# Kernel optimization log

Measured on AMD Instinct MI355X. Metric: run time of the kernel, lower is better.

## Reference

```python
import jax, jax.numpy as jnp
import numpy as np

PYR = 40000
N_PV, N_OLM, N_BIST = 2100, 1800, 1200
N_SEPT = 100
DT = 1.0
E_EXC, E_INH = 3.0, -0.5


def _sparse_uniform(key, n_out, n_in, conn, w_max, no_autapse=False):
    km, kw = jax.random.split(key)
    mask = jax.random.uniform(km, (n_out, n_in)) < conn
    w = jnp.where(mask, jax.random.uniform(kw, (n_out, n_in)) * w_max, 0.0)
    if no_autapse:
        w = w * (1.0 - jnp.eye(n_out))
    return w.astype(jnp.float32)


def setup_inputs() -> dict:
    key = jax.random.key(0)
    ks = jax.random.split(key, 24)
    inp = {}
    inp['pyr_spikes'] = jax.random.randint(ks[0], (PYR,), 0, 2, dtype=jnp.int32)
    inp['septal_gaba'] = jax.random.uniform(ks[1], (N_SEPT,), dtype=jnp.float32)
    inp['external_exc'] = jax.random.uniform(ks[2], (N_PV,), dtype=jnp.float32)
    inp['prev_pv_spikes'] = (jax.random.uniform(ks[3], (N_PV,)) < 0.1).astype(jnp.float32)
    inp['prev_olm_spikes'] = (jax.random.uniform(ks[4], (N_OLM,)) < 0.1).astype(jnp.float32)
    inp['prev_pv_v_mem'] = jax.random.uniform(ks[5], (N_PV,), dtype=jnp.float32)
    inp['pv_v'] = jax.random.uniform(ks[6], (N_PV,), dtype=jnp.float32)
    inp['olm_v'] = jax.random.uniform(ks[7], (N_OLM,), dtype=jnp.float32)
    inp['bist_v'] = jax.random.uniform(ks[8], (N_BIST,), dtype=jnp.float32)
    inp['pv_adapt'] = jnp.zeros((N_PV,), jnp.float32)
    inp['olm_adapt'] = jnp.zeros((N_OLM,), jnp.float32)
    inp['bist_adapt'] = jnp.zeros((N_BIST,), jnp.float32)
    # weights per WeightInitializer.sparse_uniform calls in __init__ (ca1_inhibitory branch)
    inp['pyr_to_pv'] = _sparse_uniform(ks[9], N_PV, PYR, 0.5, 0.0012)
    inp['pyr_to_olm'] = _sparse_uniform(ks[10], N_OLM, PYR, 0.3, 0.0006)
    inp['pyr_to_bist'] = _sparse_uniform(ks[11], N_BIST, PYR, 0.35, 0.0007)
    inp['pv_to_pyr'] = _sparse_uniform(ks[12], PYR, N_PV, 0.5, 0.003)
    inp['pv_to_pyr_gaba_b'] = _sparse_uniform(ks[13], PYR, N_PV, 0.5, 0.003 * 0.15)
    inp['olm_to_pyr'] = _sparse_uniform(ks[14], PYR, N_OLM, 0.5, 0.001)
    inp['bist_to_pyr'] = _sparse_uniform(ks[15], PYR, N_BIST, 0.55, 0.002)
    inp['pv_to_pv'] = _sparse_uniform(ks[16], N_PV, N_PV, 0.3, 0.0005, no_autapse=True)
    inp['olm_to_pv'] = _sparse_uniform(ks[17], N_PV, N_OLM, 0.2, 0.0004)
    gj = _sparse_uniform(ks[18], N_PV, N_PV, 0.5, 0.0003, no_autapse=True)
    inp['pv_gap'] = (gj + gj.T) * 0.5  # symmetrized gap junctions
    inp['septal_to_olm'] = (jnp.abs(jax.random.normal(ks[19], (N_OLM, N_SEPT))) * 0.5).astype(jnp.float32)
    return inp


def _split_exc(g, nmda_ratio=0.3):
    g = jnp.maximum(g, 0.0)  # conductances are nonnegative
    return g * (1.0 - nmda_ratio), g * nmda_ratio


def _lif_step(v, adapt, g_ampa, g_nmda, g_gaba_a, tau_mem, v_th, v_reset, tau_adapt, adapt_inc):
    # conductance-based LIF: leak toward 0 (v_rest), synaptic currents toward reversals
    i_syn = (g_ampa + g_nmda) * (E_EXC - v) + g_gaba_a * (E_INH - v)
    v_new = v + (DT / tau_mem) * (-v + i_syn)
    spk = (v_new >= (v_th + adapt)).astype(v.dtype)
    v_out = jnp.where(spk > 0, v_reset, v_new)
    adapt_new = adapt * (1.0 - DT / tau_adapt) + adapt_inc * spk
    return spk, v_out, adapt_new


def reference(pyr_spikes, septal_gaba, external_exc, prev_pv_spikes, prev_olm_spikes,
              prev_pv_v_mem, pv_v, olm_v, bist_v, pv_adapt, olm_adapt, bist_adapt,
              pyr_to_pv, pyr_to_olm, pyr_to_bist, pv_to_pyr, pv_to_pyr_gaba_b,
              olm_to_pyr, bist_to_pyr, pv_to_pv, olm_to_pv, pv_gap, septal_to_olm):
    pyr_f = pyr_spikes.astype(jnp.float32)
    pv_exc = pyr_to_pv @ pyr_f
    olm_exc = pyr_to_olm @ pyr_f
    bist_exc = pyr_to_bist @ pyr_f
    pv_exc_from_pyr = pv_exc
    ext_mean = external_exc.mean()
    pv_exc = pv_exc + ext_mean * 0.3
    olm_exc = olm_exc + ext_mean * 0.1
    bist_exc = bist_exc + ext_mean * 0.2
    olm_g_inh = septal_to_olm @ septal_gaba
    pv_lateral = pv_to_pv @ prev_pv_spikes
    olm_to_pv_inhib = olm_to_pv @ prev_olm_spikes
    pv_exc = pv_exc - pv_lateral * 0.5 - olm_to_pv_inhib * 0.3
    # gap junctions: gated by mean pyramidal drive (traced condition -> where)
    drive = pv_exc_from_pyr.mean()
    gain = jnp.where(drive > 0.01, jnp.minimum(1.0, drive / 0.1), 0.0)
    pv_gap_current = pv_gap @ prev_pv_v_mem  # v @ W.T with symmetric-ish W
    pv_exc = pv_exc + pv_gap_current * 0.05 * gain
    pv_ga, pv_gn = _split_exc(pv_exc)
    olm_ga, olm_gn = _split_exc(olm_exc)
    bi_ga, bi_gn = _split_exc(bist_exc)
    zero_pv = jnp.zeros_like(pv_v)
    zero_bi = jnp.zeros_like(bist_v)
    pv_spk, _, _ = _lif_step(pv_v, pv_adapt, pv_ga, pv_gn, zero_pv, 7.0, 2.0, 0.0, 50.0, 0.05)
    olm_spk, _, _ = _lif_step(olm_v, olm_adapt, olm_ga, olm_gn, olm_g_inh, 25.0, 1.1, 0.0, 100.0, 0.2)
    bist_spk, _, _ = _lif_step(bist_v, bist_adapt, bi_ga, bi_gn, zero_bi, 12.0, 0.9, 0.0, 60.0, 0.08)
    perisomatic = pv_to_pyr @ pv_spk
    perisomatic_gaba_b = pv_to_pyr_gaba_b @ pv_spk
    olm_dendritic = olm_to_pyr @ olm_spk
    dendritic = olm_dendritic + bist_to_pyr @ bist_spk
    return (perisomatic, perisomatic_gaba_b, dendritic, olm_dendritic, pv_spk, olm_spk, bist_spk)
```

## Files before the change

kernel.cpp:

```cpp
#include <hip/hip_runtime.h>

#define PYR 40000
#define N_PV 2100
#define N_OLM 1800
#define N_BIST 1200
#define N_SEPT 100

#define WS_PV_RAW   0
#define WS_OLM_RAW  2100
#define WS_BIST_RAW 3900
#define WS_PV_LAT   5100
#define WS_OLM_IPV  7200
#define WS_GAP      9300
#define WS_OLM_GINH 11400
#define WS_SCAL     13200

#define O_PERI 0
#define O_GABA 40000
#define O_DEND 80000
#define O_OLMD 120000
#define O_PVS  160000
#define O_OLMS 162100
#define O_BIS  163900

__device__ __forceinline__ float wave_reduce(float acc) {
    #pragma unroll
    for (int o = 32; o > 0; o >>= 1) acc += __shfl_down(acc, o, 64);
    return acc;
}

__global__ __launch_bounds__(256) void k_phase1(
    const float* __restrict__ Wpv, const float* __restrict__ Wolm,
    const float* __restrict__ Wbi, const int* __restrict__ pyr,
    float* __restrict__ ws)
{
    int b = blockIdx.x;
    const float* W;
    float* dst;
    if (b < N_PV)               { W = Wpv  + (size_t)b * PYR;                 dst = ws + WS_PV_RAW  + b; }
    else if (b < N_PV + N_OLM)  { int r = b - N_PV;         W = Wolm + (size_t)r * PYR; dst = ws + WS_OLM_RAW  + r; }
    else                        { int r = b - N_PV - N_OLM; W = Wbi  + (size_t)r * PYR; dst = ws + WS_BIST_RAW + r; }

    const float4* W4 = (const float4*)W;
    const int4*   S4 = (const int4*)pyr;
    float acc = 0.0f;
    for (int j = threadIdx.x; j < PYR / 4; j += 256) {
        float4 w = W4[j];
        int4   s = S4[j];
        acc += w.x * (float)s.x + w.y * (float)s.y + w.z * (float)s.z + w.w * (float)s.w;
    }
    acc = wave_reduce(acc);
    __shared__ float sm[4];
    int lane = threadIdx.x & 63, wv = threadIdx.x >> 6;
    if (lane == 0) sm[wv] = acc;
    __syncthreads();
    if (threadIdx.x == 0) *dst = sm[0] + sm[1] + sm[2] + sm[3];
}

__global__ __launch_bounds__(256) void k_small(
    const float* __restrict__ Wpvpv, const float* __restrict__ Wolmpv,
    const float* __restrict__ Wgap,  const float* __restrict__ Wsept,
    const float* __restrict__ prev_pv, const float* __restrict__ prev_olm,
    const float* __restrict__ prev_vm, const float* __restrict__ sept_g,
    float* __restrict__ ws)
{
    int r = blockIdx.x * 4 + (threadIdx.x >> 6);
    int lane = threadIdx.x & 63;
    const float* W; const float* v; int len4; float* dst;
    if (r < N_PV)                   { W = Wpvpv  + (size_t)r * N_PV;              v = prev_pv;  len4 = N_PV / 4;  dst = ws + WS_PV_LAT  + r; }
    else if (r < 2 * N_PV)          { int i = r - N_PV;     W = Wolmpv + (size_t)i * N_OLM;  v = prev_olm; len4 = N_OLM / 4; dst = ws + WS_OLM_IPV + i; }
    else if (r < 3 * N_PV)          { int i = r - 2 * N_PV; W = Wgap   + (size_t)i * N_PV;   v = prev_vm;  len4 = N_PV / 4;  dst = ws + WS_GAP     + i; }
    else if (r < 3 * N_PV + N_OLM)  { int i = r - 3 * N_PV; W = Wsept  + (size_t)i * N_SEPT; v = sept_g;   len4 = N_SEPT / 4; dst = ws + WS_OLM_GINH + i; }
    else return;

    const float4* W4 = (const float4*)W;
    const float4* V4 = (const float4*)v;
    float acc = 0.0f;
    for (int j = lane; j < len4; j += 64) {
        float4 w = W4[j], x = V4[j];
        acc += w.x * x.x + w.y * x.y + w.z * x.z + w.w * x.w;
    }
    acc = wave_reduce(acc);
    if (lane == 0) *dst = acc;
}

__global__ __launch_bounds__(256) void k_scal(const float* __restrict__ ext, float* __restrict__ ws)
{
    __shared__ float s1[256], s2[256];
    float a = 0.0f, b = 0.0f;
    for (int i = threadIdx.x; i < N_PV; i += 256) { a += ext[i]; b += ws[WS_PV_RAW + i]; }
    s1[threadIdx.x] = a; s2[threadIdx.x] = b;
    __syncthreads();
    for (int o = 128; o > 0; o >>= 1) {
        if (threadIdx.x < o) { s1[threadIdx.x] += s1[threadIdx.x + o]; s2[threadIdx.x] += s2[threadIdx.x + o]; }
        __syncthreads();
    }
    if (threadIdx.x == 0) {
        float ext_mean = s1[0] / (float)N_PV;
        float drive    = s2[0] / (float)N_PV;
        float gain = (drive > 0.01f) ? fminf(1.0f, drive / 0.1f) : 0.0f;
        ws[WS_SCAL]     = ext_mean;
        ws[WS_SCAL + 1] = gain;
    }
}

__global__ __launch_bounds__(256) void k_lif(
    const float* __restrict__ ws,
    const float* __restrict__ pv_v,  const float* __restrict__ olm_v,  const float* __restrict__ bist_v,
    const float* __restrict__ pv_ad, const float* __restrict__ olm_ad, const float* __restrict__ bist_ad,
    float* __restrict__ out)
{
    int t = blockIdx.x * 256 + threadIdx.x;
    float ext_mean = ws[WS_SCAL], gain = ws[WS_SCAL + 1];
    if (t < N_PV) {
        float g = ws[WS_PV_RAW + t] + ext_mean * 0.3f
                - ws[WS_PV_LAT + t] * 0.5f - ws[WS_OLM_IPV + t] * 0.3f
                + ws[WS_GAP + t] * 0.05f * gain;
        g = fmaxf(g, 0.0f);
        float ga = g * 0.7f, gn = g * 0.3f;
        float v = pv_v[t], ad = pv_ad[t];
        float isyn = (ga + gn) * (3.0f - v);
        float vn = v + (1.0f / 7.0f) * (-v + isyn);
        out[O_PVS + t] = (vn >= 2.0f + ad) ? 1.0f : 0.0f;
    } else if (t < N_PV + N_OLM) {
        int i = t - N_PV;
        float g = ws[WS_OLM_RAW + i] + ext_mean * 0.1f;
        g = fmaxf(g, 0.0f);
        float ga = g * 0.7f, gn = g * 0.3f;
        float gi = ws[WS_OLM_GINH + i];
        float v = olm_v[i], ad = olm_ad[i];
        float isyn = (ga + gn) * (3.0f - v) + gi * (-0.5f - v);
        float vn = v + (1.0f / 25.0f) * (-v + isyn);
        out[O_OLMS + i] = (vn >= 1.1f + ad) ? 1.0f : 0.0f;
    } else if (t < N_PV + N_OLM + N_BIST) {
        int i = t - N_PV - N_OLM;
        float g = ws[WS_BIST_RAW + i] + ext_mean * 0.2f;
        g = fmaxf(g, 0.0f);
        float ga = g * 0.7f, gn = g * 0.3f;
        float v = bist_v[i], ad = bist_ad[i];
        float isyn = (ga + gn) * (3.0f - v);
        float vn = v + (1.0f / 12.0f) * (-v + isyn);
        out[O_BIS + i] = (vn >= 0.9f + ad) ? 1.0f : 0.0f;
    }
}

__global__ __launch_bounds__(256) void k_phase2(
    const float* __restrict__ Wpp, const float* __restrict__ Wppb,
    const float* __restrict__ Wop, const float* __restrict__ Wbp,
    float* __restrict__ out)
{
    int r = blockIdx.x * 4 + (threadIdx.x >> 6);
    int lane = threadIdx.x & 63;
    int job = r / PYR;
    int p = r - job * PYR;
    const float* W; const float* v; int len4; float* dst;
    if (job == 0)      { W = Wpp  + (size_t)p * N_PV;   v = out + O_PVS;  len4 = N_PV / 4;   dst = out + O_PERI + p; }
    else if (job == 1) { W = Wppb + (size_t)p * N_PV;   v = out + O_PVS;  len4 = N_PV / 4;   dst = out + O_GABA + p; }
    else if (job == 2) { W = Wop  + (size_t)p * N_OLM;  v = out + O_OLMS; len4 = N_OLM / 4;  dst = out + O_OLMD + p; }
    else               { W = Wbp  + (size_t)p * N_BIST; v = out + O_BIS;  len4 = N_BIST / 4; dst = out + O_DEND + p; }

    const float4* W4 = (const float4*)W;
    const float4* V4 = (const float4*)v;
    float acc = 0.0f;
    for (int j = lane; j < len4; j += 64) {
        float4 w = W4[j], x = V4[j];
        acc += w.x * x.x + w.y * x.y + w.z * x.z + w.w * x.w;
    }
    acc = wave_reduce(acc);
    if (lane == 0) *dst = acc;
}

__global__ __launch_bounds__(256) void k_add(float* __restrict__ out)
{
    int i = blockIdx.x * 256 + threadIdx.x;
    if (i < PYR) out[O_DEND + i] += out[O_OLMD + i];
}

extern "C" void kernel_launch(void* const* d_in, const int* in_sizes, int n_in,
                              void* d_out, int out_size, void* d_ws, size_t ws_size,
                              hipStream_t stream)
{
    const int*   pyr     = (const int*)  d_in[0];
    const float* sept_g  = (const float*)d_in[1];
    const float* ext     = (const float*)d_in[2];
    const float* prev_pv = (const float*)d_in[3];
    const float* prev_olm= (const float*)d_in[4];
    const float* prev_vm = (const float*)d_in[5];
    const float* pv_v    = (const float*)d_in[6];
    const float* olm_v   = (const float*)d_in[7];
    const float* bist_v  = (const float*)d_in[8];
    const float* pv_ad   = (const float*)d_in[9];
    const float* olm_ad  = (const float*)d_in[10];
    const float* bist_ad = (const float*)d_in[11];
    const float* Wpyr_pv = (const float*)d_in[12];
    const float* Wpyr_olm= (const float*)d_in[13];
    const float* Wpyr_bi = (const float*)d_in[14];
    const float* Wpp     = (const float*)d_in[15];
    const float* Wppb    = (const float*)d_in[16];
    const float* Wop     = (const float*)d_in[17];
    const float* Wbp     = (const float*)d_in[18];
    const float* Wpvpv   = (const float*)d_in[19];
    const float* Wolmpv  = (const float*)d_in[20];
    const float* Wgap    = (const float*)d_in[21];
    const float* Wsept   = (const float*)d_in[22];

    float* ws  = (float*)d_ws;
    float* out = (float*)d_out;

    k_phase1<<<N_PV + N_OLM + N_BIST, 256, 0, stream>>>(Wpyr_pv, Wpyr_olm, Wpyr_bi, pyr, ws);
    k_small<<<(3 * N_PV + N_OLM) / 4, 256, 0, stream>>>(Wpvpv, Wolmpv, Wgap, Wsept,
                                                        prev_pv, prev_olm, prev_vm, sept_g, ws);
    k_scal<<<1, 256, 0, stream>>>(ext, ws);
    k_lif<<<(N_PV + N_OLM + N_BIST + 255) / 256, 256, 0, stream>>>(
        ws, pv_v, olm_v, bist_v, pv_ad, olm_ad, bist_ad, out);
    k_phase2<<<(4 * PYR) / 4, 256, 0, stream>>>(Wpp, Wppb, Wop, Wbp, out);
    k_add<<<(PYR + 255) / 256, 256, 0, stream>>>(out);
}
```

Baseline: 368.7 us.

## Fuse launches, merge dendritic dot products, and use nontemporal weight loads

Merges the large pyramidal-input matvec kernel and the small recurrent matvec kernel into one launch. The scalar-mean reduction moves into the LIF kernel, where every block recomputes it redundantly. Phase 2 now computes the OLM and bistratified dot products in the same wave, so the separate add kernel goes away. Weight streams use nontemporal loads to avoid polluting cache. This removes three launches and an extra pass over the dendritic output, at the cost of redundant reductions and more divergent block types.

```diff
diff --git a/kernel.cpp b/kernel.cpp
--- a/kernel.cpp
+++ b/kernel.cpp
@@ -13,7 +13,6 @@
 #define WS_OLM_IPV  7200
 #define WS_GAP      9300
 #define WS_OLM_GINH 11400
-#define WS_SCAL     13200
 
 #define O_PERI 0
 #define O_GABA 40000
@@ -23,122 +22,113 @@
 #define O_OLMS 162100
 #define O_BIS  163900
 
+typedef float f4 __attribute__((ext_vector_type(4)));
+typedef int   i4 __attribute__((ext_vector_type(4)));
+
+__device__ __forceinline__ f4 ntload(const f4* p) { return __builtin_nontemporal_load(p); }
+
 __device__ __forceinline__ float wave_reduce(float acc) {
     #pragma unroll
     for (int o = 32; o > 0; o >>= 1) acc += __shfl_down(acc, o, 64);
     return acc;
 }
 
-__global__ __launch_bounds__(256) void k_phase1(
+#define P1_BLOCKS (N_PV + N_OLM + N_BIST)
+#define SMALL_BLOCKS ((3 * N_PV + N_OLM + 3) / 4)
+__global__ __launch_bounds__(256) void k_big(
     const float* __restrict__ Wpv, const float* __restrict__ Wolm,
     const float* __restrict__ Wbi, const int* __restrict__ pyr,
-    float* __restrict__ ws)
-{
-    int b = blockIdx.x;
-    const float* W;
-    float* dst;
-    if (b < N_PV)               { W = Wpv  + (size_t)b * PYR;                 dst = ws + WS_PV_RAW  + b; }
-    else if (b < N_PV + N_OLM)  { int r = b - N_PV;         W = Wolm + (size_t)r * PYR; dst = ws + WS_OLM_RAW  + r; }
-    else                        { int r = b - N_PV - N_OLM; W = Wbi  + (size_t)r * PYR; dst = ws + WS_BIST_RAW + r; }
-
-    const float4* W4 = (const float4*)W;
-    const int4*   S4 = (const int4*)pyr;
-    float acc = 0.0f;
-    for (int j = threadIdx.x; j < PYR / 4; j += 256) {
-        float4 w = W4[j];
-        int4   s = S4[j];
-        acc += w.x * (float)s.x + w.y * (float)s.y + w.z * (float)s.z + w.w * (float)s.w;
-    }
-    acc = wave_reduce(acc);
-    __shared__ float sm[4];
-    int lane = threadIdx.x & 63, wv = threadIdx.x >> 6;
-    if (lane == 0) sm[wv] = acc;
-    __syncthreads();
-    if (threadIdx.x == 0) *dst = sm[0] + sm[1] + sm[2] + sm[3];
-}
-
-__global__ __launch_bounds__(256) void k_small(
     const float* __restrict__ Wpvpv, const float* __restrict__ Wolmpv,
     const float* __restrict__ Wgap,  const float* __restrict__ Wsept,
     const float* __restrict__ prev_pv, const float* __restrict__ prev_olm,
     const float* __restrict__ prev_vm, const float* __restrict__ sept_g,
     float* __restrict__ ws)
 {
-    int r = blockIdx.x * 4 + (threadIdx.x >> 6);
+    int b = blockIdx.x;
+    if (b < P1_BLOCKS) {
+        const float* W; float* dst;
+        if (b < N_PV)               { W = Wpv  + (size_t)b * PYR;                   dst = ws + WS_PV_RAW  + b; }
+        else if (b < N_PV + N_OLM)  { int r = b - N_PV;         W = Wolm + (size_t)r * PYR; dst = ws + WS_OLM_RAW  + r; }
+        else                        { int r = b - N_PV - N_OLM; W = Wbi  + (size_t)r * PYR; dst = ws + WS_BIST_RAW + r; }
+
+        const f4* W4 = (const f4*)W;
+        const i4* S4 = (const i4*)pyr;
+        float acc = 0.0f;
+        for (int j = threadIdx.x; j < PYR / 4; j += 256) {
+            f4 w = ntload(W4 + j);
+            i4 s = S4[j];
+            acc += w.x * (float)s.x + w.y * (float)s.y + w.z * (float)s.z + w.w * (float)s.w;
+        }
+        acc = wave_reduce(acc);
+        __shared__ float sm[4];
+        int lane = threadIdx.x & 63, wv = threadIdx.x >> 6;
+        if (lane == 0) sm[wv] = acc;
+        __syncthreads();
+        if (threadIdx.x == 0) *dst = sm[0] + sm[1] + sm[2] + sm[3];
+        return;
+    }
+    int r = (b - P1_BLOCKS) * 4 + (threadIdx.x >> 6);
     int lane = threadIdx.x & 63;
     const float* W; const float* v; int len4; float* dst;
-    if (r < N_PV)                   { W = Wpvpv  + (size_t)r * N_PV;              v = prev_pv;  len4 = N_PV / 4;  dst = ws + WS_PV_LAT  + r; }
-    else if (r < 2 * N_PV)          { int i = r - N_PV;     W = Wolmpv + (size_t)i * N_OLM;  v = prev_olm; len4 = N_OLM / 4; dst = ws + WS_OLM_IPV + i; }
-    else if (r < 3 * N_PV)          { int i = r - 2 * N_PV; W = Wgap   + (size_t)i * N_PV;   v = prev_vm;  len4 = N_PV / 4;  dst = ws + WS_GAP     + i; }
+    if (r < N_PV)                   { W = Wpvpv  + (size_t)r * N_PV;               v = prev_pv;  len4 = N_PV / 4;   dst = ws + WS_PV_LAT  + r; }
+    else if (r < 2 * N_PV)          { int i = r - N_PV;     W = Wolmpv + (size_t)i * N_OLM;  v = prev_olm; len4 = N_OLM / 4;  dst = ws + WS_OLM_IPV + i; }
+    else if (r < 3 * N_PV)          { int i = r - 2 * N_PV; W = Wgap   + (size_t)i * N_PV;   v = prev_vm;  len4 = N_PV / 4;   dst = ws + WS_GAP     + i; }
     else if (r < 3 * N_PV + N_OLM)  { int i = r - 3 * N_PV; W = Wsept  + (size_t)i * N_SEPT; v = sept_g;   len4 = N_SEPT / 4; dst = ws + WS_OLM_GINH + i; }
     else return;
 
-    const float4* W4 = (const float4*)W;
-    const float4* V4 = (const float4*)v;
+    const f4* W4 = (const f4*)W;
+    const f4* V4 = (const f4*)v;
     float acc = 0.0f;
     for (int j = lane; j < len4; j += 64) {
-        float4 w = W4[j], x = V4[j];
+        f4 w = ntload(W4 + j), x = V4[j];
         acc += w.x * x.x + w.y * x.y + w.z * x.z + w.w * x.w;
     }
     acc = wave_reduce(acc);
     if (lane == 0) *dst = acc;
 }
 
-__global__ __launch_bounds__(256) void k_scal(const float* __restrict__ ext, float* __restrict__ ws)
+__global__ __launch_bounds__(256) void k_lif(
+    const float* __restrict__ ws, const float* __restrict__ ext,
+    const float* __restrict__ pv_v,  const float* __restrict__ olm_v,  const float* __restrict__ bist_v,
+    const float* __restrict__ pv_ad, const float* __restrict__ olm_ad, const float* __restrict__ bist_ad,
+    float* __restrict__ out)
 {
     __shared__ float s1[256], s2[256];
-    float a = 0.0f, b = 0.0f;
-    for (int i = threadIdx.x; i < N_PV; i += 256) { a += ext[i]; b += ws[WS_PV_RAW + i]; }
-    s1[threadIdx.x] = a; s2[threadIdx.x] = b;
+    float a = 0.0f, bsum = 0.0f;
+    for (int i = threadIdx.x; i < N_PV; i += 256) { a += ext[i]; bsum += ws[WS_PV_RAW + i]; }
+    s1[threadIdx.x] = a; s2[threadIdx.x] = bsum;
     __syncthreads();
     for (int o = 128; o > 0; o >>= 1) {
         if (threadIdx.x < o) { s1[threadIdx.x] += s1[threadIdx.x + o]; s2[threadIdx.x] += s2[threadIdx.x + o]; }
         __syncthreads();
     }
-    if (threadIdx.x == 0) {
-        float ext_mean = s1[0] / (float)N_PV;
-        float drive    = s2[0] / (float)N_PV;
-        float gain = (drive > 0.01f) ? fminf(1.0f, drive / 0.1f) : 0.0f;
-        ws[WS_SCAL]     = ext_mean;
-        ws[WS_SCAL + 1] = gain;
-    }
-}
-
-__global__ __launch_bounds__(256) void k_lif(
-    const float* __restrict__ ws,
-    const float* __restrict__ pv_v,  const float* __restrict__ olm_v,  const float* __restrict__ bist_v,
-    const float* __restrict__ pv_ad, const float* __restrict__ olm_ad, const float* __restrict__ bist_ad,
-    float* __restrict__ out)
-{
+    float ext_mean = s1[0] / (float)N_PV;
+    float drive    = s2[0] / (float)N_PV;
+    float gain = (drive > 0.01f) ? fminf(1.0f, drive / 0.1f) : 0.0f;
+
     int t = blockIdx.x * 256 + threadIdx.x;
-    float ext_mean = ws[WS_SCAL], gain = ws[WS_SCAL + 1];
     if (t < N_PV) {
         float g = ws[WS_PV_RAW + t] + ext_mean * 0.3f
                 - ws[WS_PV_LAT + t] * 0.5f - ws[WS_OLM_IPV + t] * 0.3f
                 + ws[WS_GAP + t] * 0.05f * gain;
         g = fmaxf(g, 0.0f);
-        float ga = g * 0.7f, gn = g * 0.3f;
         float v = pv_v[t], ad = pv_ad[t];
-        float isyn = (ga + gn) * (3.0f - v);
+        float isyn = g * (3.0f - v);
         float vn = v + (1.0f / 7.0f) * (-v + isyn);
         out[O_PVS + t] = (vn >= 2.0f + ad) ? 1.0f : 0.0f;
     } else if (t < N_PV + N_OLM) {
         int i = t - N_PV;
-        float g = ws[WS_OLM_RAW + i] + ext_mean * 0.1f;
-        g = fmaxf(g, 0.0f);
-        float ga = g * 0.7f, gn = g * 0.3f;
+        float g = fmaxf(ws[WS_OLM_RAW + i] + ext_mean * 0.1f, 0.0f);
         float gi = ws[WS_OLM_GINH + i];
         float v = olm_v[i], ad = olm_ad[i];
-        float isyn = (ga + gn) * (3.0f - v) + gi * (-0.5f - v);
+        float isyn = g * (3.0f - v) + gi * (-0.5f - v);
         float vn = v + (1.0f / 25.0f) * (-v + isyn);
         out[O_OLMS + i] = (vn >= 1.1f + ad) ? 1.0f : 0.0f;
     } else if (t < N_PV + N_OLM + N_BIST) {
         int i = t - N_PV - N_OLM;
-        float g = ws[WS_BIST_RAW + i] + ext_mean * 0.2f;
-        g = fmaxf(g, 0.0f);
-        float ga = g * 0.7f, gn = g * 0.3f;
+        float g = fmaxf(ws[WS_BIST_RAW + i] + ext_mean * 0.2f, 0.0f);
         float v = bist_v[i], ad = bist_ad[i];
-        float isyn = (ga + gn) * (3.0f - v);
+        float isyn = g * (3.0f - v);
         float vn = v + (1.0f / 12.0f) * (-v + isyn);
         out[O_BIS + i] = (vn >= 0.9f + ad) ? 1.0f : 0.0f;
     }
@@ -153,27 +143,39 @@
     int lane = threadIdx.x & 63;
     int job = r / PYR;
     int p = r - job * PYR;
-    const float* W; const float* v; int len4; float* dst;
-    if (job == 0)      { W = Wpp  + (size_t)p * N_PV;   v = out + O_PVS;  len4 = N_PV / 4;   dst = out + O_PERI + p; }
-    else if (job == 1) { W = Wppb + (size_t)p * N_PV;   v = out + O_PVS;  len4 = N_PV / 4;   dst = out + O_GABA + p; }
-    else if (job == 2) { W = Wop  + (size_t)p * N_OLM;  v = out + O_OLMS; len4 = N_OLM / 4;  dst = out + O_OLMD + p; }
-    else               { W = Wbp  + (size_t)p * N_BIST; v = out + O_BIS;  len4 = N_BIST / 4; dst = out + O_DEND + p; }
-
-    const float4* W4 = (const float4*)W;
-    const float4* V4 = (const float4*)v;
-    float acc = 0.0f;
-    for (int j = lane; j < len4; j += 64) {
-        float4 w = W4[j], x = V4[j];
-        acc += w.x * x.x + w.y * x.y + w.z * x.z + w.w * x.w;
-    }
-    acc = wave_reduce(acc);
-    if (lane == 0) *dst = acc;
-}
-
-__global__ __launch_bounds__(256) void k_add(float* __restrict__ out)
-{
-    int i = blockIdx.x * 256 + threadIdx.x;
-    if (i < PYR) out[O_DEND + i] += out[O_OLMD + i];
+
+    if (job < 2) {
+        const float* W = (job == 0 ? Wpp : Wppb) + (size_t)p * N_PV;
+        const f4* W4 = (const f4*)W;
+        const f4* V4 = (const f4*)(out + O_PVS);
+        float acc = 0.0f;
+        for (int j = lane; j < N_PV / 4; j += 64) {
+            f4 w = ntload(W4 + j), x = V4[j];
+            acc += w.x * x.x + w.y * x.y + w.z * x.z + w.w * x.w;
+        }
+        acc = wave_reduce(acc);
+        if (lane == 0) out[(job == 0 ? O_PERI : O_GABA) + p] = acc;
+    } else {
+        const f4* Wo4 = (const f4*)(Wop + (size_t)p * N_OLM);
+        const f4* Wb4 = (const f4*)(Wbp + (size_t)p * N_BIST);
+        const f4* Vo4 = (const f4*)(out + O_OLMS);
+        const f4* Vb4 = (const f4*)(out + O_BIS);
+        float ao = 0.0f, ab = 0.0f;
+        for (int j = lane; j < N_OLM / 4; j += 64) {
+            f4 w = ntload(Wo4 + j), x = Vo4[j];
+            ao += w.x * x.x + w.y * x.y + w.z * x.z + w.w * x.w;
+        }
+        for (int j = lane; j < N_BIST / 4; j += 64) {
+            f4 w = ntload(Wb4 + j), x = Vb4[j];
+            ab += w.x * x.x + w.y * x.y + w.z * x.z + w.w * x.w;
+        }
+        ao = wave_reduce(ao);
+        ab = wave_reduce(ab);
+        if (lane == 0) {
+            out[O_OLMD + p] = ao;
+            out[O_DEND + p] = ao + ab;
+        }
+    }
 }
 
 extern "C" void kernel_launch(void* const* d_in, const int* in_sizes, int n_in,
@@ -207,12 +209,11 @@
     float* ws  = (float*)d_ws;
     float* out = (float*)d_out;
 
-    k_phase1<<<N_PV + N_OLM + N_BIST, 256, 0, stream>>>(Wpyr_pv, Wpyr_olm, Wpyr_bi, pyr, ws);
-    k_small<<<(3 * N_PV + N_OLM) / 4, 256, 0, stream>>>(Wpvpv, Wolmpv, Wgap, Wsept,
-                                                        prev_pv, prev_olm, prev_vm, sept_g, ws);
-    k_scal<<<1, 256, 0, stream>>>(ext, ws);
+    k_big<<<P1_BLOCKS + SMALL_BLOCKS, 256, 0, stream>>>(
+        Wpyr_pv, Wpyr_olm, Wpyr_bi, pyr,
+        Wpvpv, Wolmpv, Wgap, Wsept,
+        prev_pv, prev_olm, prev_vm, sept_g, ws);
     k_lif<<<(N_PV + N_OLM + N_BIST + 255) / 256, 256, 0, stream>>>(
-        ws, pv_v, olm_v, bist_v, pv_ad, olm_ad, bist_ad, out);
-    k_phase2<<<(4 * PYR) / 4, 256, 0, stream>>>(Wpp, Wppb, Wop, Wbp, out);
-    k_add<<<(PYR + 255) / 256, 256, 0, stream>>>(out);
-}
+        ws, ext, pv_v, olm_v, bist_v, pv_ad, olm_ad, bist_ad, out);
+    k_phase2<<<(3 * PYR) / 4, 256, 0, stream>>>(Wpp, Wppb, Wop, Wbp, out);
+}
```

Measured after the change: 334.2 us. -9.3%, faster.
